# Optimization experiments

Measured on AMD Instinct MI355X. Metric: run time of the kernel, lower is better.

The kernel has to match this reference:

```python
import jax, jax.numpy as jnp
import numpy as np

EPS = 1e-5
H = 12  # num_heads

def ste_sign(x):
    # forward: sign(x) in {-1,+1}; backward: grad passes where |x|<1 (clip STE)
    c = jnp.clip(x, -1.0, 1.0)
    s = jnp.where(x >= 0, 1.0, -1.0).astype(x.dtype)
    return c + jax.lax.stop_gradient(s - c)

def bin_w(w):
    # adaptive per-output-channel scaling: alpha = mean|w| (detached), weight = alpha*sign(w)
    alpha = jax.lax.stop_gradient(jnp.mean(jnp.abs(w), axis=1, keepdims=True))
    return alpha * ste_sign(w)

def layernorm(x, g, b):
    mu = jnp.mean(x, axis=-1, keepdims=True)
    var = jnp.var(x, axis=-1, keepdims=True)
    return (x - mu) * jax.lax.rsqrt(var + EPS) * g + b

def setup_inputs():
    key = jax.random.key(0)
    ks = jax.random.split(key, 6)
    B, N, C, hid = 8, 1024, 768, 3072
    s = 0.02
    return {
        "x": jax.random.normal(ks[0], (B, N, C), jnp.float32),
        "ln1_g": jnp.ones((C,), jnp.float32),
        "ln1_b": jnp.zeros((C,), jnp.float32),
        "w_qkv": jax.random.normal(ks[1], (3 * C, C), jnp.float32) * s,
        "w_proj": jax.random.normal(ks[2], (C, C), jnp.float32) * s,
        "b_proj": jnp.zeros((C,), jnp.float32),
        "ls1_g": 1e-5 * jnp.ones((C,), jnp.float32),
        "ln2_g": jnp.ones((C,), jnp.float32),
        "ln2_b": jnp.zeros((C,), jnp.float32),
        "w_fc1": jax.random.normal(ks[3], (hid, C), jnp.float32) * s,
        "b_fc1": jnp.zeros((hid,), jnp.float32),
        "w_fc2": jax.random.normal(ks[4], (C, hid), jnp.float32) * s,
        "b_fc2": jnp.zeros((C,), jnp.float32),
        "ls2_g": 1e-5 * jnp.ones((C,), jnp.float32),
    }

def reference(x, ln1_g, ln1_b, w_qkv, w_proj, b_proj, ls1_g, ln2_g, ln2_b, w_fc1, b_fc1, w_fc2, b_fc2, ls2_g):
    B, N, C = x.shape
    hd = C // H
    scale = hd ** -0.5
    # --- binarized attention ---
    h = layernorm(x, ln1_g, ln1_b)
    qkv = jnp.einsum('bnc,oc->bno', ste_sign(h), bin_w(w_qkv))        # 1w1a qkv proj
    qkv = qkv.reshape(B, N, 3, H, hd).transpose(2, 0, 3, 1, 4)        # [3,B,H,N,hd]
    bqkv = ste_sign(qkv)                                              # BinaryQuantizer
    q, k, v = bqkv[0], bqkv[1], bqkv[2]
    attn = jnp.einsum('bhnd,bhmd->bhnm', q, k) * scale                # [B,H,N,N]
    sm = jax.nn.softmax(attn, axis=-1)
    abin = (attn > 0).astype(x.dtype)                                 # SoftmaxBinaryQuantizer fwd value
    attn_eff = sm + jax.lax.stop_gradient(abin - sm)                  # STE: fwd=binary, bwd=softmax
    o = jnp.einsum('bhnm,bhmd->bhnd', attn_eff, v)
    o = o.transpose(0, 2, 1, 3).reshape(B, N, C)
    o = jnp.einsum('bnc,oc->bno', ste_sign(o), bin_w(w_proj)) + b_proj
    x = x + ls1_g * o
    # --- binary MLP (1-bit weight, 32-bit activation) ---
    h2 = layernorm(x, ln2_g, ln2_b)
    m = jax.nn.gelu(jnp.einsum('bnc,hc->bnh', h2, bin_w(w_fc1)) + b_fc1, approximate=False)
    m = jnp.einsum('bnh,ch->bnc', m, bin_w(w_fc2)) + b_fc2
    return x + ls2_g * m
```

## Files before the change

kernel.cpp:

```cpp
#include <hip/hip_runtime.h>

#define NTOK 8192
#define CDIM 768
#define HIDD 3072
#define NQKV 2304
#define SEQL 1024
#define NHEAD 12

typedef int i32x4 __attribute__((ext_vector_type(4)));
typedef float f32x4 __attribute__((ext_vector_type(4)));
typedef signed char sc16 __attribute__((ext_vector_type(16)));

__device__ __forceinline__ void gload_lds16(const void* g, void* l) {
    __builtin_amdgcn_global_load_lds(
        (const __attribute__((address_space(1))) unsigned int*)g,
        (__attribute__((address_space(3))) unsigned int*)l, 16, 0, 0);
}

__global__ void sign_w_kernel(const float* __restrict__ w, signed char* __restrict__ ws, int n) {
    int i = blockIdx.x * blockDim.x + threadIdx.x;
    int stride = gridDim.x * blockDim.x;
    for (; i < n; i += stride)
        ws[i] = (w[i] >= 0.0f) ? 1 : -1;
}

template<bool PERM>
__global__ void __launch_bounds__(256) signalpha_kernel(const float* __restrict__ w,
                                                        signed char* __restrict__ ws,
                                                        float* __restrict__ alpha, int K) {
    int row = blockIdx.x;
    const float* wr = w + (size_t)row * K;
    signed char* wsr = ws + (size_t)row * K;
    float s = 0.f;
    for (int i = threadIdx.x; i < K; i += 256) {
        float v = wr[i];
        int ip = PERM ? ((i & ~63) | (((i & 15) << 2) | ((i >> 4) & 3))) : i;
        wsr[ip] = (v >= 0.f) ? 1 : -1;
        s += fabsf(v);
    }
    for (int off = 32; off > 0; off >>= 1) s += __shfl_down(s, off);
    __shared__ float red[4];
    if ((threadIdx.x & 63) == 0) red[threadIdx.x >> 6] = s;
    __syncthreads();
    if (threadIdx.x == 0) alpha[row] = (red[0] + red[1] + red[2] + red[3]) / (float)K;
}

__global__ void __launch_bounds__(256) ln_sign_kernel(const float* __restrict__ x, const float* __restrict__ g,
                                                      const float* __restrict__ b, signed char* __restrict__ out) {
    int row = blockIdx.x;
    const float* xr = x + (size_t)row * CDIM;
    float v0 = xr[threadIdx.x], v1 = xr[threadIdx.x + 256], v2 = xr[threadIdx.x + 512];
    float s = v0 + v1 + v2, s2 = v0 * v0 + v1 * v1 + v2 * v2;
    for (int off = 32; off > 0; off >>= 1) { s += __shfl_down(s, off); s2 += __shfl_down(s2, off); }
    __shared__ float red[8];
    if ((threadIdx.x & 63) == 0) { red[threadIdx.x >> 6] = s; red[4 + (threadIdx.x >> 6)] = s2; }
    __syncthreads();
    float ts = red[0] + red[1] + red[2] + red[3];
    float t2 = red[4] + red[5] + red[6] + red[7];
    float mu = ts * (1.0f / CDIM);
    float var = t2 * (1.0f / CDIM) - mu * mu;
    float rstd = rsqrtf(var + 1e-5f);
    signed char* orow = out + (size_t)row * CDIM;
    float vv[3] = {v0, v1, v2};
#pragma unroll
    for (int p = 0; p < 3; p++) {
        int i = threadIdx.x + p * 256;
        float val = (vv[p] - mu) * rstd * g[i] + b[i];
        orow[i] = (val >= 0.f) ? 1 : -1;
    }
}

__global__ void __launch_bounds__(256) ln2q_kernel(const float* __restrict__ x, const float* __restrict__ g,
                                                   const float* __restrict__ b, signed char* __restrict__ out,
                                                   float* __restrict__ rowscale) {
    int row = blockIdx.x;
    const float* xr = x + (size_t)row * CDIM;
    float v0 = xr[threadIdx.x], v1 = xr[threadIdx.x + 256], v2 = xr[threadIdx.x + 512];
    float s = v0 + v1 + v2, s2 = v0 * v0 + v1 * v1 + v2 * v2;
    for (int off = 32; off > 0; off >>= 1) { s += __shfl_down(s, off); s2 += __shfl_down(s2, off); }
    __shared__ float red[8];
    __shared__ float redm[4];
    if ((threadIdx.x & 63) == 0) { red[threadIdx.x >> 6] = s; red[4 + (threadIdx.x >> 6)] = s2; }
    __syncthreads();
    float ts = red[0] + red[1] + red[2] + red[3];
    float t2 = red[4] + red[5] + red[6] + red[7];
    float mu = ts * (1.0f / CDIM);
    float var = t2 * (1.0f / CDIM) - mu * mu;
    float rstd = rsqrtf(var + 1e-5f);
    float a0 = (v0 - mu) * rstd * g[threadIdx.x] + b[threadIdx.x];
    float a1 = (v1 - mu) * rstd * g[threadIdx.x + 256] + b[threadIdx.x + 256];
    float a2v = (v2 - mu) * rstd * g[threadIdx.x + 512] + b[threadIdx.x + 512];
    float mx = fmaxf(fabsf(a0), fmaxf(fabsf(a1), fabsf(a2v)));
    for (int off = 32; off > 0; off >>= 1) mx = fmaxf(mx, __shfl_down(mx, off));
    if ((threadIdx.x & 63) == 0) redm[threadIdx.x >> 6] = mx;
    __syncthreads();
    float rmax = fmaxf(fmaxf(redm[0], redm[1]), fmaxf(redm[2], redm[3]));
    rmax = fmaxf(rmax, 1e-20f);
    float inv = 127.f / rmax;
    signed char* orow = out + (size_t)row * CDIM;
    orow[threadIdx.x]       = (signed char)__float2int_rn(a0 * inv);
    orow[threadIdx.x + 256] = (signed char)__float2int_rn(a1 * inv);
    orow[threadIdx.x + 512] = (signed char)__float2int_rn(a2v * inv);
    if (threadIdx.x == 0) rowscale[row] = rmax * (1.f / 127.f);
}

enum { EPI_GELU = 2, EPI_QKV = 3 };
#define MSCALE_INV 16.0f

template<int EPI, int BN>
__global__ void __launch_bounds__(256) gemm_i8(
    const signed char* __restrict__ A, const signed char* __restrict__ B,
    int M, int N, int K,
    const float* __restrict__ alpha, const float* __restrict__ bias,
    const float* __restrict__ rowscale,
    signed char* __restrict__ outB, signed char* __restrict__ vtB)
{
    __shared__ __align__(16) char lds_raw[3 * (128 + BN) * 64];
    auto As = (signed char (*)[128][64])lds_raw;
    auto Bs = (signed char (*)[BN][64])(lds_raw + 3 * 128 * 64);

    const int tid = threadIdx.x, ln = tid & 63, w = tid >> 6;
    const int wm = w >> 1, wn = w & 1;
    const int lq = ln & 15, khi = ln >> 4;
    constexpr int NF = BN / 32;
    constexpr int L = (BN == 128) ? 4 : 3;

    const int nwg = gridDim.x * gridDim.y;
    const int id = blockIdx.y * gridDim.x + blockIdx.x;
    const int nid = (id & 7) * (nwg >> 3) + (id >> 3);
    const int bxs = nid % gridDim.x, bys = nid / gridDim.x;
    const int bm = bys * 128, bn = bxs * BN;

    const i32x4 iz = {0, 0, 0, 0};
    i32x4 acc[4][NF];
#pragma unroll
    for (int m = 0; m < 4; m++)
#pragma unroll
        for (int n = 0; n < NF; n++) acc[m][n] = iz;

    const int srow = tid >> 2, scol = (tid & 3) * 16;
    const int ssrc = ((tid & 3) ^ ((srow >> 1) & 3)) * 16;
    const int sa = 16 * (khi ^ ((lq >> 1) & 3));

    auto STAGE = [&](int p, int k0) {
        gload_lds16(A + (size_t)(bm + srow) * K + k0 + ssrc, &As[p][srow][scol]);
        gload_lds16(A + (size_t)(bm + 64 + srow) * K + k0 + ssrc, &As[p][64 + srow][scol]);
        gload_lds16(B + (size_t)(bn + srow) * K + k0 + ssrc, &Bs[p][srow][scol]);
        if constexpr (BN == 128)
            gload_lds16(B + (size_t)(bn + 64 + srow) * K + k0 + ssrc, &Bs[p][64 + srow][scol]);
    };
    auto COMPUTE = [&](int p, bool prefetch, int knext) {
        i32x4 aF[4], bF[NF];
#pragma unroll
        for (int m = 0; m < 4; m++) aF[m] = *(const i32x4*)&As[p][wm * 64 + m * 16 + lq][sa];
#pragma unroll
        for (int n = 0; n < NF; n++) bF[n] = *(const i32x4*)&Bs[p][wn * (BN / 2) + n * 16 + lq][sa];
        if (prefetch) STAGE((p + 2) % 3, knext);
        __builtin_amdgcn_s_setprio(1);
#pragma unroll
        for (int m = 0; m < 4; m++)
#pragma unroll
            for (int n = 0; n < NF; n++)
                acc[m][n] = __builtin_amdgcn_mfma_i32_16x16x64_i8(aF[m], bF[n], acc[m][n], 0, 0, 0);
        __builtin_amdgcn_s_setprio(0);
    };

    const int nst = K >> 6;
    STAGE(0, 0);
    STAGE(1, 64);
#pragma unroll 1
    for (int t = 0; t < nst - 1; t++) {
        asm volatile("s_waitcnt vmcnt(%0)" :: "n"(L) : "memory");
        __builtin_amdgcn_s_barrier();
        COMPUTE(t % 3, t + 2 < nst, (t + 2) << 6);
    }
    asm volatile("s_waitcnt vmcnt(0)" ::: "memory");
    __builtin_amdgcn_s_barrier();
    COMPUTE((nst - 1) % 3, false, 0);

    const int r0 = bm + wm * 64, c0loc = wn * (BN / 2);

    if constexpr (EPI == EPI_GELU) {
        float al[NF], bi[NF];
#pragma unroll
        for (int n = 0; n < NF; n++) {
            int c = bn + c0loc + n * 16 + lq;
            al[n] = alpha[c]; bi[n] = bias[c];
        }
#pragma unroll
        for (int m = 0; m < 4; m++)
#pragma unroll
            for (int i = 0; i < 4; i++) {
                int r = r0 + m * 16 + khi * 4 + i;
                float rs = rowscale[r];
                unsigned pk = 0;
#pragma unroll
                for (int n = 0; n < NF; n++) {
                    float t = al[n] * ((float)acc[m][n][i] * rs) + bi[n];
                    float y2 = 1.5957691f * t + 0.07135481f * t * t * t;
                    float ge = t * __builtin_amdgcn_rcpf(1.0f + __expf(-y2));
                    float qf = fminf(fmaxf(ge * MSCALE_INV, -127.f), 127.f);
                    pk |= (unsigned)(unsigned char)(signed char)__float2int_rn(qf) << (8 * n);
                }
                *(unsigned*)(outB + (size_t)r * N + bn + c0loc + lq * 4) = pk;
            }
    } else {
        if (bn < 1536) {
#pragma unroll
            for (int m = 0; m < 4; m++)
#pragma unroll
                for (int i = 0; i < 4; i++) {
                    int r = r0 + m * 16 + khi * 4 + i;
                    unsigned pk = 0;
#pragma unroll
                    for (int n = 0; n < NF; n++)
                        pk |= (unsigned)(unsigned char)(signed char)((acc[m][n][i] >= 0) ? 1 : -1) << (8 * n);
                    *(unsigned*)(outB + (size_t)r * 1536 + bn + c0loc + lq * 4) = pk;
                }
        } else {
#pragma unroll
            for (int m = 0; m < 4; m++)
#pragma unroll
                for (int n = 0; n < NF; n++) {
                    int cg = bn + c0loc + n * 16 + lq - 1536;
                    int hh = cg >> 6, dd = cg & 63;
                    int rb = r0 + m * 16 + khi * 4;
                    unsigned pk = 0;
#pragma unroll
                    for (int i = 0; i < 4; i++)
                        pk |= (unsigned)(unsigned char)(signed char)((acc[m][n][i] >= 0) ? 1 : -1) << (8 * i);
                    *(unsigned*)(vtB + (((size_t)(rb >> 10) * NHEAD + hh) * 64 + dd) * SEQL + (rb & 1023)) = pk;
                }
        }
    }
}

__global__ void __launch_bounds__(256) gemm_resid(
    const signed char* __restrict__ A, const signed char* __restrict__ B,
    int N, int K,
    const float* __restrict__ alpha, const float* __restrict__ bias,
    const float* __restrict__ ls, const float* __restrict__ resid,
    float ascale, float* __restrict__ outF)
{
    __shared__ __align__(16) char lds_raw[24576];
    auto As = (signed char (*)[64][64])lds_raw;
    auto Bs = (signed char (*)[64][64])(lds_raw + 3 * 64 * 64);

    const int tid = threadIdx.x, ln = tid & 63, w = tid >> 6;
    const int wm = w >> 1, wn = w & 1;
    const int lq = ln & 15, khi = ln >> 4;

    const int nwg = gridDim.x * gridDim.y;
    const int id = blockIdx.y * gridDim.x + blockIdx.x;
    const int nid = (id & 7) * (nwg >> 3) + (id >> 3);
    const int bxs = nid % gridDim.x, bys = nid / gridDim.x;
    const int bm = bys * 64, bn = bxs * 64;

    const int ec4 = (tid & 15) * 4, erow0 = tid >> 4;
    f32x4 a4 = *(const f32x4*)&alpha[bn + ec4];
    f32x4 b4 = *(const f32x4*)&bias[bn + ec4];
    f32x4 l4 = *(const f32x4*)&ls[bn + ec4];
    f32x4 r4[4];
#pragma unroll
    for (int p = 0; p < 4; p++)
        r4[p] = *(const f32x4*)&resid[(size_t)(bm + erow0 + p * 16) * N + bn + ec4];

    const i32x4 iz = {0, 0, 0, 0};
    i32x4 acc[2][2] = {{iz, iz}, {iz, iz}};

    const int srow = tid >> 2, scol = (tid & 3) * 16;
    const int ssrc = ((tid & 3) ^ ((srow >> 1) & 3)) * 16;
    const int sa = 16 * (khi ^ ((lq >> 1) & 3));

    auto STAGE = [&](int p, int k0) {
        gload_lds16(A + (size_t)(bm + srow) * K + k0 + ssrc, &As[p][srow][scol]);
        gload_lds16(B + (size_t)(bn + srow) * K + k0 + ssrc, &Bs[p][srow][scol]);
    };
    auto COMPUTE = [&](int p, bool prefetch, int knext) {
        i32x4 aF[2], bF[2];
#pragma unroll
        for (int m = 0; m < 2; m++) aF[m] = *(const i32x4*)&As[p][wm * 32 + m * 16 + lq][sa];
#pragma unroll
        for (int n = 0; n < 2; n++) bF[n] = *(const i32x4*)&Bs[p][wn * 32 + n * 16 + lq][sa];
        if (prefetch) STAGE((p + 2) % 3, knext);
        __builtin_amdgcn_s_setprio(1);
#pragma unroll
        for (int m = 0; m < 2; m++)
#pragma unroll
            for (int n = 0; n < 2; n++)
                acc[m][n] = __builtin_amdgcn_mfma_i32_16x16x64_i8(aF[m], bF[n], acc[m][n], 0, 0, 0);
        __builtin_amdgcn_s_setprio(0);
    };

    const int nst = K >> 6;
    STAGE(0, 0);
    STAGE(1, 64);
#pragma unroll 1
    for (int t = 0; t < nst - 1; t++) {
        asm volatile("s_waitcnt vmcnt(2)" ::: "memory");
        __builtin_amdgcn_s_barrier();
        COMPUTE(t % 3, t + 2 < nst, (t + 2) << 6);
    }
    asm volatile("s_waitcnt vmcnt(0)" ::: "memory");
    __builtin_amdgcn_s_barrier();
    COMPUTE((nst - 1) % 3, false, 0);

    __syncthreads();
    float (*Cf)[68] = (float (*)[68])lds_raw;
#pragma unroll
    for (int m = 0; m < 2; m++)
#pragma unroll
        for (int n = 0; n < 2; n++)
#pragma unroll
            for (int i = 0; i < 4; i++)
                Cf[wm * 32 + m * 16 + khi * 4 + i][wn * 32 + n * 16 + lq] =
                    (float)acc[m][n][i] * ascale;
    __syncthreads();
#pragma unroll
    for (int p = 0; p < 4; p++) {
        f32x4 v4 = *(const f32x4*)&Cf[erow0 + p * 16][ec4];
        f32x4 o4 = r4[p] + l4 * (a4 * v4 + b4);
        *(f32x4*)&outF[(size_t)(bm + erow0 + p * 16) * N + bn + ec4] = o4;
    }
}

__global__ void __launch_bounds__(256) attn_v2(const signed char* __restrict__ qk,
                                               const signed char* __restrict__ vt,
                                               signed char* __restrict__ a2) {
    const int id = blockIdx.x;
    const int nid = (id & 7) * 96 + (id >> 3);
    const int bh = nid >> 3, qb = nid & 7;
    const int b = bh / NHEAD, h = bh % NHEAD;
    const int tid = threadIdx.x, ln = tid & 63, w = tid >> 6;
    const int lq = ln & 15, khi = ln >> 4;

    __shared__ signed char Ks[64][80];
    __shared__ signed char Vts[64][80];
    __shared__ signed char Pw[4][32][80];

    const size_t tokbase = (size_t)b * SEQL;
    const int q0 = qb * 128 + w * 32;
    const int str = tid >> 2, stc = (tid & 3) * 16;
    const size_t vtrow = ((size_t)bh * 64 + str) * SEQL;

    i32x4 qfrag[2];
#pragma unroll
    for (int qf = 0; qf < 2; qf++)
        qfrag[qf] = *(const i32x4*)(qk + (tokbase + q0 + qf * 16 + lq) * 1536 + h * 64 + khi * 16);

    const i32x4 iz = {0, 0, 0, 0};
    i32x4 o[2][4];
#pragma unroll
    for (int qf = 0; qf < 2; qf++)
#pragma unroll
        for (int df = 0; df < 4; df++) o[qf][df] = iz;

    auto LOADJ = [&](int j, sc16& kr, sc16& vr) {
        kr = *(const sc16*)(qk + (tokbase + j * 64 + str) * 1536 + 768 + h * 64 + stc);
        vr = *(const sc16*)(vt + vtrow + j * 64 + stc);
    };
    auto STORE = [&](const sc16& kr, const sc16& vr) {
        *(sc16*)&Ks[str][stc] = kr;
        *(sc16*)&Vts[str][stc] = vr;
    };
    auto COMPUTE = [&]() {
        i32x4 kfrag[4];
#pragma unroll
        for (int kf = 0; kf < 4; kf++)
            kfrag[kf] = *(const i32x4*)&Ks[kf * 16 + lq][khi * 16];
#pragma unroll
        for (int kf = 0; kf < 4; kf++) {
#pragma unroll
            for (int qf = 0; qf < 2; qf++) {
                i32x4 st = __builtin_amdgcn_mfma_i32_16x16x64_i8(kfrag[kf], qfrag[qf], iz, 0, 0, 0);
                unsigned pb = (st[0] > 0 ? 1u : 0u) | (st[1] > 0 ? 0x100u : 0u) |
                              (st[2] > 0 ? 0x10000u : 0u) | (st[3] > 0 ? 0x1000000u : 0u);
                *(unsigned*)&Pw[w][qf * 16 + lq][kf * 16 + khi * 4] = pb;
            }
        }
        i32x4 pa[2];
#pragma unroll
        for (int qf = 0; qf < 2; qf++)
            pa[qf] = *(const i32x4*)&Pw[w][qf * 16 + lq][khi * 16];
#pragma unroll
        for (int df = 0; df < 4; df++) {
            i32x4 vfr = *(const i32x4*)&Vts[df * 16 + lq][khi * 16];
#pragma unroll
            for (int qf = 0; qf < 2; qf++)
                o[qf][df] = __builtin_amdgcn_mfma_i32_16x16x64_i8(pa[qf], vfr, o[qf][df], 0, 0, 0);
        }
    };

    sc16 ka, va, kb, vb;
    LOADJ(0, ka, va);
#pragma unroll 1
    for (int jj = 0; jj < 16; jj += 2) {
        __syncthreads();
        STORE(ka, va);
        __syncthreads();
        LOADJ(jj + 1, kb, vb);
        COMPUTE();
        __syncthreads();
        STORE(kb, vb);
        __syncthreads();
        if (jj + 2 < 16) LOADJ(jj + 2, ka, va);
        COMPUTE();
    }

#pragma unroll
    for (int qf = 0; qf < 2; qf++)
#pragma unroll
        for (int i = 0; i < 4; i++) {
            int qrow = q0 + qf * 16 + khi * 4 + i;
            unsigned pk = 0;
#pragma unroll
            for (int df = 0; df < 4; df++)
                pk |= (unsigned)(unsigned char)(signed char)((o[qf][df][i] >= 0) ? 1 : -1) << (8 * df);
            *(unsigned*)(a2 + (tokbase + qrow) * CDIM + h * 64 + lq * 4) = pk;
        }
}

static const size_t OFF_WQKV  = 0;
static const size_t OFF_WPROJ = 1769472;
static const size_t OFF_WFC1  = 2359296;
static const size_t OFF_WFC2  = 4718592;
static const size_t OFF_APROJ = 7077888;
static const size_t OFF_AFC1  = 7080960;
static const size_t OFF_AFC2  = 7093248;
static const size_t OFF_H2SC  = 7096320;
static const size_t OFF_QK    = 7129088;
static const size_t OFF_VT    = 19712000;
static const size_t OFF_A2    = 26003456;
static const size_t OFF_A1    = 32294912;
static const size_t OFF_M1    = 38586368;
static const size_t OFF_H2    = 63752192;

extern "C" void kernel_launch(void* const* d_in, const int* in_sizes, int n_in,
                              void* d_out, int out_size, void* d_ws, size_t ws_size,
                              hipStream_t stream) {
    const float* x      = (const float*)d_in[0];
    const float* ln1_g  = (const float*)d_in[1];
    const float* ln1_b  = (const float*)d_in[2];
    const float* w_qkv  = (const float*)d_in[3];
    const float* w_proj = (const float*)d_in[4];
    const float* b_proj = (const float*)d_in[5];
    const float* ls1_g  = (const float*)d_in[6];
    const float* ln2_g  = (const float*)d_in[7];
    const float* ln2_b  = (const float*)d_in[8];
    const float* w_fc1  = (const float*)d_in[9];
    const float* b_fc1  = (const float*)d_in[10];
    const float* w_fc2  = (const float*)d_in[11];
    const float* b_fc2  = (const float*)d_in[12];
    const float* ls2_g  = (const float*)d_in[13];
    float* out = (float*)d_out;

    char* ws = (char*)d_ws;
    signed char* wqkv_s  = (signed char*)(ws + OFF_WQKV);
    signed char* wproj_s = (signed char*)(ws + OFF_WPROJ);
    signed char* wfc1_s  = (signed char*)(ws + OFF_WFC1);
    signed char* wfc2_s  = (signed char*)(ws + OFF_WFC2);
    float* a_proj  = (float*)(ws + OFF_APROJ);
    float* a_fc1   = (float*)(ws + OFF_AFC1);
    float* a_fc2   = (float*)(ws + OFF_AFC2);
    float* h2scale = (float*)(ws + OFF_H2SC);
    signed char* qk   = (signed char*)(ws + OFF_QK);
    signed char* vt   = (signed char*)(ws + OFF_VT);
    signed char* a2   = (signed char*)(ws + OFF_A2);
    signed char* a1   = (signed char*)(ws + OFF_A1);
    signed char* m1   = (signed char*)(ws + OFF_M1);
    signed char* h2   = (signed char*)(ws + OFF_H2);

    sign_w_kernel<<<512, 256, 0, stream>>>(w_qkv, wqkv_s, NQKV * CDIM);
    signalpha_kernel<true><<<CDIM, 256, 0, stream>>>(w_proj, wproj_s, a_proj, CDIM);
    signalpha_kernel<false><<<HIDD, 256, 0, stream>>>(w_fc1,  wfc1_s,  a_fc1,  CDIM);
    signalpha_kernel<true><<<CDIM, 256, 0, stream>>>(w_fc2,  wfc2_s,  a_fc2,  HIDD);

    ln_sign_kernel<<<NTOK, 256, 0, stream>>>(x, ln1_g, ln1_b, a1);

    gemm_i8<EPI_QKV, 128><<<dim3(NQKV / 128, NTOK / 128), 256, 0, stream>>>(
        a1, wqkv_s, NTOK, NQKV, CDIM, nullptr, nullptr, nullptr, qk, vt);

    attn_v2<<<768, 256, 0, stream>>>(qk, vt, a2);

    gemm_resid<<<dim3(CDIM / 64, NTOK / 64), 256, 0, stream>>>(
        a2, wproj_s, CDIM, CDIM, a_proj, b_proj, ls1_g, x, 1.0f, out);

    ln2q_kernel<<<NTOK, 256, 0, stream>>>(out, ln2_g, ln2_b, h2, h2scale);

    gemm_i8<EPI_GELU, 128><<<dim3(HIDD / 128, NTOK / 128), 256, 0, stream>>>(
        h2, wfc1_s, NTOK, HIDD, CDIM, a_fc1, b_fc1, h2scale, m1, nullptr);

    gemm_resid<<<dim3(CDIM / 64, NTOK / 64), 256, 0, stream>>>(
        m1, wfc2_s, CDIM, HIDD, a_fc2, b_fc2, ls2_g, out, 1.0f / MSCALE_INV, out);
}
```

Measured before the change: 181.9 us.

## Enlarge GEMM tiles, deepen pipeline, split epilogues into fused row kernels

```diff
diff --git a/kernel.cpp b/kernel.cpp
--- a/kernel.cpp
+++ b/kernel.cpp
@@ -70,13 +70,25 @@
     }
 }
 
-__global__ void __launch_bounds__(256) ln2q_kernel(const float* __restrict__ x, const float* __restrict__ g,
-                                                   const float* __restrict__ b, signed char* __restrict__ out,
-                                                   float* __restrict__ rowscale) {
+__global__ void __launch_bounds__(256) proj_ln_fuse(
+    const float* __restrict__ acc, const float* __restrict__ x,
+    const float* __restrict__ ap, const float* __restrict__ bp, const float* __restrict__ ls1,
+    const float* __restrict__ g2, const float* __restrict__ b2,
+    float* __restrict__ x1out, signed char* __restrict__ h2, float* __restrict__ rowscale) {
     int row = blockIdx.x;
+    const float* ar = acc + (size_t)row * CDIM;
     const float* xr = x + (size_t)row * CDIM;
-    float v0 = xr[threadIdx.x], v1 = xr[threadIdx.x + 256], v2 = xr[threadIdx.x + 512];
-    float s = v0 + v1 + v2, s2 = v0 * v0 + v1 * v1 + v2 * v2;
+    float* x1r = x1out + (size_t)row * CDIM;
+    float v[3];
+    float s = 0.f, s2 = 0.f;
+#pragma unroll
+    for (int p = 0; p < 3; p++) {
+        int i = threadIdx.x + p * 256;
+        float t = xr[i] + ls1[i] * (ap[i] * ar[i] + bp[i]);
+        x1r[i] = t;
+        v[p] = t;
+        s += t; s2 += t * t;
+    }
     for (int off = 32; off > 0; off >>= 1) { s += __shfl_down(s, off); s2 += __shfl_down(s2, off); }
     __shared__ float red[8];
     __shared__ float redm[4];
@@ -87,56 +99,75 @@
     float mu = ts * (1.0f / CDIM);
     float var = t2 * (1.0f / CDIM) - mu * mu;
     float rstd = rsqrtf(var + 1e-5f);
-    float a0 = (v0 - mu) * rstd * g[threadIdx.x] + b[threadIdx.x];
-    float a1 = (v1 - mu) * rstd * g[threadIdx.x + 256] + b[threadIdx.x + 256];
-    float a2v = (v2 - mu) * rstd * g[threadIdx.x + 512] + b[threadIdx.x + 512];
-    float mx = fmaxf(fabsf(a0), fmaxf(fabsf(a1), fabsf(a2v)));
+    float a[3];
+    float mx = 0.f;
+#pragma unroll
+    for (int p = 0; p < 3; p++) {
+        int i = threadIdx.x + p * 256;
+        a[p] = (v[p] - mu) * rstd * g2[i] + b2[i];
+        mx = fmaxf(mx, fabsf(a[p]));
+    }
     for (int off = 32; off > 0; off >>= 1) mx = fmaxf(mx, __shfl_down(mx, off));
     if ((threadIdx.x & 63) == 0) redm[threadIdx.x >> 6] = mx;
     __syncthreads();
     float rmax = fmaxf(fmaxf(redm[0], redm[1]), fmaxf(redm[2], redm[3]));
     rmax = fmaxf(rmax, 1e-20f);
     float inv = 127.f / rmax;
-    signed char* orow = out + (size_t)row * CDIM;
-    orow[threadIdx.x]       = (signed char)__float2int_rn(a0 * inv);
-    orow[threadIdx.x + 256] = (signed char)__float2int_rn(a1 * inv);
-    orow[threadIdx.x + 512] = (signed char)__float2int_rn(a2v * inv);
+    signed char* orow = h2 + (size_t)row * CDIM;
+#pragma unroll
+    for (int p = 0; p < 3; p++)
+        orow[threadIdx.x + p * 256] = (signed char)__float2int_rn(a[p] * inv);
     if (threadIdx.x == 0) rowscale[row] = rmax * (1.f / 127.f);
+}
+
+__global__ void __launch_bounds__(256) fc2_fuse(
+    const float* __restrict__ acc, const float* __restrict__ af2,
+    const float* __restrict__ bf2, const float* __restrict__ ls2, float* __restrict__ out) {
+    int n4 = NTOK * CDIM / 4;
+    int stride = gridDim.x * 256;
+    for (int i4 = blockIdx.x * 256 + threadIdx.x; i4 < n4; i4 += stride) {
+        int c4 = (i4 << 2) % CDIM;
+        f32x4 a = *(const f32x4*)&af2[c4];
+        f32x4 b = *(const f32x4*)&bf2[c4];
+        f32x4 l = *(const f32x4*)&ls2[c4];
+        f32x4 vacc = *(const f32x4*)&acc[(size_t)i4 * 4];
+        f32x4 o = *(const f32x4*)&out[(size_t)i4 * 4];
+        o = o + l * (a * vacc + b);
+        *(f32x4*)&out[(size_t)i4 * 4] = o;
+    }
 }
 
 enum { EPI_GELU = 2, EPI_QKV = 3 };
 #define MSCALE_INV 16.0f
 
-template<int EPI, int BN>
-__global__ void __launch_bounds__(256) gemm_i8(
+template<int EPI>
+__global__ void __launch_bounds__(512, 4) gemm_i8(
     const signed char* __restrict__ A, const signed char* __restrict__ B,
     int M, int N, int K,
     const float* __restrict__ alpha, const float* __restrict__ bias,
     const float* __restrict__ rowscale,
     signed char* __restrict__ outB, signed char* __restrict__ vtB)
 {
-    __shared__ __align__(16) char lds_raw[3 * (128 + BN) * 64];
-    auto As = (signed char (*)[128][64])lds_raw;
-    auto Bs = (signed char (*)[BN][64])(lds_raw + 3 * 128 * 64);
+    __shared__ __align__(16) char lds_raw[3 * (256 + 128) * 64];
+    auto As = (signed char (*)[256][64])lds_raw;
+    auto Bs = (signed char (*)[128][64])(lds_raw + 3 * 256 * 64);
 
     const int tid = threadIdx.x, ln = tid & 63, w = tid >> 6;
     const int wm = w >> 1, wn = w & 1;
     const int lq = ln & 15, khi = ln >> 4;
-    constexpr int NF = BN / 32;
-    constexpr int L = (BN == 128) ? 4 : 3;
 
     const int nwg = gridDim.x * gridDim.y;
     const int id = blockIdx.y * gridDim.x + blockIdx.x;
     const int nid = (id & 7) * (nwg >> 3) + (id >> 3);
     const int bxs = nid % gridDim.x, bys = nid / gridDim.x;
-    const int bm = bys * 128, bn = bxs * BN;
+    const int bm = bys * 256, bn = bxs * 128;
 
     const i32x4 iz = {0, 0, 0, 0};
-    i32x4 acc[4][NF];
+    i32x4 acc[4][4];
 #pragma unroll
     for (int m = 0; m < 4; m++)
 #pragma unroll
-        for (int n = 0; n < NF; n++) acc[m][n] = iz;
+        for (int n = 0; n < 4; n++) acc[m][n] = iz;
 
     const int srow = tid >> 2, scol = (tid & 3) * 16;
     const int ssrc = ((tid & 3) ^ ((srow >> 1) & 3)) * 16;
@@ -144,23 +175,21 @@
 
     auto STAGE = [&](int p, int k0) {
         gload_lds16(A + (size_t)(bm + srow) * K + k0 + ssrc, &As[p][srow][scol]);
-        gload_lds16(A + (size_t)(bm + 64 + srow) * K + k0 + ssrc, &As[p][64 + srow][scol]);
+        gload_lds16(A + (size_t)(bm + 128 + srow) * K + k0 + ssrc, &As[p][128 + srow][scol]);
         gload_lds16(B + (size_t)(bn + srow) * K + k0 + ssrc, &Bs[p][srow][scol]);
-        if constexpr (BN == 128)
-            gload_lds16(B + (size_t)(bn + 64 + srow) * K + k0 + ssrc, &Bs[p][64 + srow][scol]);
     };
     auto COMPUTE = [&](int p, bool prefetch, int knext) {
-        i32x4 aF[4], bF[NF];
+        i32x4 aF[4], bF[4];
 #pragma unroll
         for (int m = 0; m < 4; m++) aF[m] = *(const i32x4*)&As[p][wm * 64 + m * 16 + lq][sa];
 #pragma unroll
-        for (int n = 0; n < NF; n++) bF[n] = *(const i32x4*)&Bs[p][wn * (BN / 2) + n * 16 + lq][sa];
+        for (int n = 0; n < 4; n++) bF[n] = *(const i32x4*)&Bs[p][wn * 64 + n * 16 + lq][sa];
         if (prefetch) STAGE((p + 2) % 3, knext);
         __builtin_amdgcn_s_setprio(1);
 #pragma unroll
         for (int m = 0; m < 4; m++)
 #pragma unroll
-            for (int n = 0; n < NF; n++)
+            for (int n = 0; n < 4; n++)
                 acc[m][n] = __builtin_amdgcn_mfma_i32_16x16x64_i8(aF[m], bF[n], acc[m][n], 0, 0, 0);
         __builtin_amdgcn_s_setprio(0);
     };
@@ -170,22 +199,25 @@
     STAGE(1, 64);
 #pragma unroll 1
     for (int t = 0; t < nst - 1; t++) {
-        asm volatile("s_waitcnt vmcnt(%0)" :: "n"(L) : "memory");
+        asm volatile("s_waitcnt vmcnt(3)" ::: "memory");
+        asm volatile("s_waitcnt lgkmcnt(0)" ::: "memory");
         __builtin_amdgcn_s_barrier();
         COMPUTE(t % 3, t + 2 < nst, (t + 2) << 6);
     }
     asm volatile("s_waitcnt vmcnt(0)" ::: "memory");
+    asm volatile("s_waitcnt lgkmcnt(0)" ::: "memory");
     __builtin_amdgcn_s_barrier();
     COMPUTE((nst - 1) % 3, false, 0);
 
-    const int r0 = bm + wm * 64, c0loc = wn * (BN / 2);
+    const int r0 = bm + wm * 64;
+    const int c0 = bn + wn * 64;
 
     if constexpr (EPI == EPI_GELU) {
-        float al[NF], bi[NF];
-#pragma unroll
-        for (int n = 0; n < NF; n++) {
-            int c = bn + c0loc + n * 16 + lq;
-            al[n] = alpha[c]; bi[n] = bias[c];
+        float al[4], bi[4];
+#pragma unroll
+        for (int n = 0; n < 4; n++) {
+            al[n] = alpha[c0 + n * 16 + lq];
+            bi[n] = bias[c0 + n * 16 + lq];
         }
 #pragma unroll
         for (int m = 0; m < 4; m++)
@@ -195,17 +227,17 @@
                 float rs = rowscale[r];
                 unsigned pk = 0;
 #pragma unroll
-                for (int n = 0; n < NF; n++) {
+                for (int n = 0; n < 4; n++) {
                     float t = al[n] * ((float)acc[m][n][i] * rs) + bi[n];
                     float y2 = 1.5957691f * t + 0.07135481f * t * t * t;
                     float ge = t * __builtin_amdgcn_rcpf(1.0f + __expf(-y2));
                     float qf = fminf(fmaxf(ge * MSCALE_INV, -127.f), 127.f);
                     pk |= (unsigned)(unsigned char)(signed char)__float2int_rn(qf) << (8 * n);
                 }
-                *(unsigned*)(outB + (size_t)r * N + bn + c0loc + lq * 4) = pk;
+                *(unsigned*)(outB + (size_t)r * N + c0 + lq * 4) = pk;
             }
     } else {
-        if (bn < 1536) {
+        if (c0 < 1536) {
 #pragma unroll
             for (int m = 0; m < 4; m++)
 #pragma unroll
@@ -213,16 +245,16 @@
                     int r = r0 + m * 16 + khi * 4 + i;
                     unsigned pk = 0;
 #pragma unroll
-                    for (int n = 0; n < NF; n++)
+                    for (int n = 0; n < 4; n++)
                         pk |= (unsigned)(unsigned char)(signed char)((acc[m][n][i] >= 0) ? 1 : -1) << (8 * n);
-                    *(unsigned*)(outB + (size_t)r * 1536 + bn + c0loc + lq * 4) = pk;
+                    *(unsigned*)(outB + (size_t)r * 1536 + c0 + lq * 4) = pk;
                 }
         } else {
 #pragma unroll
             for (int m = 0; m < 4; m++)
 #pragma unroll
-                for (int n = 0; n < NF; n++) {
-                    int cg = bn + c0loc + n * 16 + lq - 1536;
+                for (int n = 0; n < 4; n++) {
+                    int cg = c0 + n * 16 + lq - 1536;
                     int hh = cg >> 6, dd = cg & 63;
                     int rb = r0 + m * 16 + khi * 4;
                     unsigned pk = 0;
@@ -235,16 +267,13 @@
     }
 }
 
-__global__ void __launch_bounds__(256) gemm_resid(
+__global__ void __launch_bounds__(256) gemm_acc(
     const signed char* __restrict__ A, const signed char* __restrict__ B,
-    int N, int K,
-    const float* __restrict__ alpha, const float* __restrict__ bias,
-    const float* __restrict__ ls, const float* __restrict__ resid,
-    float ascale, float* __restrict__ outF)
+    int N, int K, float ascale, float* __restrict__ outF)
 {
-    __shared__ __align__(16) char lds_raw[24576];
-    auto As = (signed char (*)[64][64])lds_raw;
-    auto Bs = (signed char (*)[64][64])(lds_raw + 3 * 64 * 64);
+    __shared__ __align__(16) char lds_raw[4 * (128 + 64) * 64];
+    auto As = (signed char (*)[128][64])lds_raw;
+    auto Bs = (signed char (*)[64][64])(lds_raw + 4 * 128 * 64);
 
     const int tid = threadIdx.x, ln = tid & 63, w = tid >> 6;
     const int wm = w >> 1, wn = w & 1;
@@ -254,19 +283,14 @@
     const int id = blockIdx.y * gridDim.x + blockIdx.x;
     const int nid = (id & 7) * (nwg >> 3) + (id >> 3);
     const int bxs = nid % gridDim.x, bys = nid / gridDim.x;
-    const int bm = bys * 64, bn = bxs * 64;
-
-    const int ec4 = (tid & 15) * 4, erow0 = tid >> 4;
-    f32x4 a4 = *(const f32x4*)&alpha[bn + ec4];
-    f32x4 b4 = *(const f32x4*)&bias[bn + ec4];
-    f32x4 l4 = *(const f32x4*)&ls[bn + ec4];
-    f32x4 r4[4];
-#pragma unroll
-    for (int p = 0; p < 4; p++)
-        r4[p] = *(const f32x4*)&resid[(size_t)(bm + erow0 + p * 16) * N + bn + ec4];
+    const int bm = bys * 128, bn = bxs * 64;
 
     const i32x4 iz = {0, 0, 0, 0};
-    i32x4 acc[2][2] = {{iz, iz}, {iz, iz}};
+    i32x4 acc[4][2];
+#pragma unroll
+    for (int m = 0; m < 4; m++)
+#pragma unroll
+        for (int n = 0; n < 2; n++) acc[m][n] = iz;
 
     const int srow = tid >> 2, scol = (tid & 3) * 16;
     const int ssrc = ((tid & 3) ^ ((srow >> 1) & 3)) * 16;
@@ -274,18 +298,19 @@
 
     auto STAGE = [&](int p, int k0) {
         gload_lds16(A + (size_t)(bm + srow) * K + k0 + ssrc, &As[p][srow][scol]);
+        gload_lds16(A + (size_t)(bm + 64 + srow) * K + k0 + ssrc, &As[p][64 + srow][scol]);
         gload_lds16(B + (size_t)(bn + srow) * K + k0 + ssrc, &Bs[p][srow][scol]);
     };
     auto COMPUTE = [&](int p, bool prefetch, int knext) {
-        i32x4 aF[2], bF[2];
-#pragma unroll
-        for (int m = 0; m < 2; m++) aF[m] = *(const i32x4*)&As[p][wm * 32 + m * 16 + lq][sa];
+        i32x4 aF[4], bF[2];
+#pragma unroll
+        for (int m = 0; m < 4; m++) aF[m] = *(const i32x4*)&As[p][wm * 64 + m * 16 + lq][sa];
 #pragma unroll
         for (int n = 0; n < 2; n++) bF[n] = *(const i32x4*)&Bs[p][wn * 32 + n * 16 + lq][sa];
-        if (prefetch) STAGE((p + 2) % 3, knext);
+        if (prefetch) STAGE((p + 3) & 3, knext);
         __builtin_amdgcn_s_setprio(1);
 #pragma unroll
-        for (int m = 0; m < 2; m++)
+        for (int m = 0; m < 4; m++)
 #pragma unroll
             for (int n = 0; n < 2; n++)
                 acc[m][n] = __builtin_amdgcn_mfma_i32_16x16x64_i8(aF[m], bF[n], acc[m][n], 0, 0, 0);
@@ -295,32 +320,35 @@
     const int nst = K >> 6;
     STAGE(0, 0);
     STAGE(1, 64);
+    STAGE(2, 128);
 #pragma unroll 1
-    for (int t = 0; t < nst - 1; t++) {
-        asm volatile("s_waitcnt vmcnt(2)" ::: "memory");
+    for (int t = 0; t < nst; t++) {
+        int rem = nst - 1 - t;
+        if (rem >= 2)      asm volatile("s_waitcnt vmcnt(6)" ::: "memory");
+        else if (rem == 1) asm volatile("s_waitcnt vmcnt(3)" ::: "memory");
+        else               asm volatile("s_waitcnt vmcnt(0)" ::: "memory");
+        asm volatile("s_waitcnt lgkmcnt(0)" ::: "memory");
         __builtin_amdgcn_s_barrier();
-        COMPUTE(t % 3, t + 2 < nst, (t + 2) << 6);
-    }
-    asm volatile("s_waitcnt vmcnt(0)" ::: "memory");
-    __builtin_amdgcn_s_barrier();
-    COMPUTE((nst - 1) % 3, false, 0);
+        COMPUTE(t & 3, t + 3 < nst, (t + 3) << 6);
+    }
 
     __syncthreads();
     float (*Cf)[68] = (float (*)[68])lds_raw;
 #pragma unroll
-    for (int m = 0; m < 2; m++)
+    for (int m = 0; m < 4; m++)
 #pragma unroll
         for (int n = 0; n < 2; n++)
 #pragma unroll
             for (int i = 0; i < 4; i++)
-                Cf[wm * 32 + m * 16 + khi * 4 + i][wn * 32 + n * 16 + lq] =
+                Cf[wm * 64 + m * 16 + khi * 4 + i][wn * 32 + n * 16 + lq] =
                     (float)acc[m][n][i] * ascale;
     __syncthreads();
 #pragma unroll
-    for (int p = 0; p < 4; p++) {
-        f32x4 v4 = *(const f32x4*)&Cf[erow0 + p * 16][ec4];
-        f32x4 o4 = r4[p] + l4 * (a4 * v4 + b4);
-        *(f32x4*)&outF[(size_t)(bm + erow0 + p * 16) * N + bn + ec4] = o4;
+    for (int p = 0; p < 8; p++) {
+        int idx = p * 256 + tid;
+        int row = idx >> 4, c4 = (idx & 15) * 4;
+        f32x4 v4 = *(const f32x4*)&Cf[row][c4];
+        *(f32x4*)&outF[(size_t)(bm + row) * N + bn + c4] = v4;
     }
 }
 
@@ -430,10 +458,11 @@
 static const size_t OFF_H2SC  = 7096320;
 static const size_t OFF_QK    = 7129088;
 static const size_t OFF_VT    = 19712000;
-static const size_t OFF_A2    = 26003456;
-static const size_t OFF_A1    = 32294912;
+static const size_t OFF_A1    = 26003456;
+static const size_t OFF_A2    = 32294912;
 static const size_t OFF_M1    = 38586368;
 static const size_t OFF_H2    = 63752192;
+static const size_t OFF_CACC  = OFF_QK;
 
 extern "C" void kernel_launch(void* const* d_in, const int* in_sizes, int n_in,
                               void* d_out, int out_size, void* d_ws, size_t ws_size,
@@ -465,10 +494,11 @@
     float* h2scale = (float*)(ws + OFF_H2SC);
     signed char* qk   = (signed char*)(ws + OFF_QK);
     signed char* vt   = (signed char*)(ws + OFF_VT);
+    signed char* a1   = (signed char*)(ws + OFF_A1);
     signed char* a2   = (signed char*)(ws + OFF_A2);
-    signed char* a1   = (signed char*)(ws + OFF_A1);
     signed char* m1   = (signed char*)(ws + OFF_M1);
     signed char* h2   = (signed char*)(ws + OFF_H2);
+    float* cacc = (float*)(ws + OFF_CACC);
 
     sign_w_kernel<<<512, 256, 0, stream>>>(w_qkv, wqkv_s, NQKV * CDIM);
     signalpha_kernel<true><<<CDIM, 256, 0, stream>>>(w_proj, wproj_s, a_proj, CDIM);
@@ -477,19 +507,22 @@
 
     ln_sign_kernel<<<NTOK, 256, 0, stream>>>(x, ln1_g, ln1_b, a1);
 
-    gemm_i8<EPI_QKV, 128><<<dim3(NQKV / 128, NTOK / 128), 256, 0, stream>>>(
+    gemm_i8<EPI_QKV><<<dim3(NQKV / 128, NTOK / 256), 512, 0, stream>>>(
         a1, wqkv_s, NTOK, NQKV, CDIM, nullptr, nullptr, nullptr, qk, vt);
 
     attn_v2<<<768, 256, 0, stream>>>(qk, vt, a2);
 
-    gemm_resid<<<dim3(CDIM / 64, NTOK / 64), 256, 0, stream>>>(
-        a2, wproj_s, CDIM, CDIM, a_proj, b_proj, ls1_g, x, 1.0f, out);
-
-    ln2q_kernel<<<NTOK, 256, 0, stream>>>(out, ln2_g, ln2_b, h2, h2scale);
-
-    gemm_i8<EPI_GELU, 128><<<dim3(HIDD / 128, NTOK / 128), 256, 0, stream>>>(
+    gemm_acc<<<dim3(CDIM / 64, NTOK / 128), 256, 0, stream>>>(
+        a2, wproj_s, CDIM, CDIM, 1.0f, cacc);
+
+    proj_ln_fuse<<<NTOK, 256, 0, stream>>>(cacc, x, a_proj, b_proj, ls1_g,
+                                           ln2_g, ln2_b, out, h2, h2scale);
+
+    gemm_i8<EPI_GELU><<<dim3(HIDD / 128, NTOK / 256), 512, 0, stream>>>(
         h2, wfc1_s, NTOK, HIDD, CDIM, a_fc1, b_fc1, h2scale, m1, nullptr);
 
-    gemm_resid<<<dim3(CDIM / 64, NTOK / 64), 256, 0, stream>>>(
-        m1, wfc2_s, CDIM, HIDD, a_fc2, b_fc2, ls2_g, out, 1.0f / MSCALE_INV, out);
-}
+    gemm_acc<<<dim3(CDIM / 64, NTOK / 128), 256, 0, stream>>>(
+        m1, wfc2_s, CDIM, HIDD, 1.0f / MSCALE_INV, cacc);
+
+    fc2_fuse<<<2048, 256, 0, stream>>>(cacc, a_fc2, b_fc2, ls2_g, out);
+}
```

Measured after the change: 186.6 us. 1.03x slower.
